# Kernel optimization log

Hardware: AMD Instinct MI355X
Metric: run time of the kernel (lower is better)

The kernel has to match this reference:

```python
import jax, jax.numpy as jnp
import numpy as np

N, L, P = 32, 512, 256
H, E = 8, 128          # n_head, n_emb; d_model = H*E = 1024
NEG = -1e20            # self.eps2 mask fill


def gelu(v):
    # torch F.gelu default = exact erf gelu
    return jax.nn.gelu(v, approximate=False)


def setup_inputs() -> dict:
    key = jax.random.key(0)
    ks = jax.random.split(key, 10)
    s = 0.05
    x = jax.random.normal(ks[0], (N, L, H * E), dtype=jnp.float32)
    hyper_adj = (jax.random.uniform(ks[1], (N, L, P)) < 0.1).astype(jnp.float32)
    W1 = jax.random.normal(ks[2], (E, E), dtype=jnp.float32) * s
    b1 = jax.random.normal(ks[3], (E,), dtype=jnp.float32) * s
    W2 = jax.random.normal(ks[4], (E,), dtype=jnp.float32) * s
    b2 = jax.random.normal(ks[5], (), dtype=jnp.float32) * s
    W3 = jax.random.normal(ks[6], (E, E), dtype=jnp.float32) * s
    b3 = jax.random.normal(ks[7], (E,), dtype=jnp.float32) * s
    W4 = jax.random.normal(ks[8], (2 * E,), dtype=jnp.float32) * s
    b4 = jax.random.normal(ks[9], (), dtype=jnp.float32) * s
    return {"x": x, "hyper_adj": hyper_adj, "W1": W1, "b1": b1, "W2": W2,
            "b2": b2, "W3": W3, "b3": b3, "W4": W4, "b4": b4}


def reference(x, hyper_adj, W1, b1, W2, b2, W3, b3, W4, b4):
    n, l, d = x.shape
    # (N, H, L, E)
    xh = x.reshape(n, l, H, E).transpose(0, 2, 1, 3)
    xh = jnp.einsum('nhle,ef->nhlf', xh, W1) + b1              # hyper_linear1
    mask = hyper_adj[:, None, :, :] != 0.0                      # (N,1,L,P), bcast over H
    # node -> edge attention: score per node broadcast over P, masked, softmax over heads (dim=1)
    xv = gelu(xh) @ W2 + b2                                     # (N,H,L)  hyper_linear2
    x_value = jnp.where(mask, xv[..., None], NEG)               # (N,H,L,P)
    att_edge = jax.nn.softmax(x_value, axis=1)
    hyper_edge = gelu(jnp.einsum('nhlp,nhle->nhpe', att_edge, xh))
    hyper_edge = jnp.einsum('nhpe,ef->nhpf', hyper_edge, W3) + b3  # hyper_linear3
    # edge -> node attention; linear4(gelu(cat(he, x))) decomposed (gelu elementwise)
    a_edge = gelu(hyper_edge) @ W4[:E]                          # (N,H,P)
    a_node = gelu(xh) @ W4[E:]                                  # (N,H,L)
    e_values = a_node[:, :, :, None] + a_edge[:, :, None, :] + b4  # (N,H,L,P)
    e_values = jnp.where(mask, e_values, NEG)
    att_node = jax.nn.softmax(e_values, axis=1)
    x_nodes = jnp.einsum('nhlp,nhpe->nhle', att_node, hyper_edge)
    out = gelu(x_nodes).transpose(0, 2, 1, 3).reshape(n, l, d)
    # scatter overwrite: nodes in no hyperedge keep their input
    no_edge = (jnp.sum(hyper_adj, axis=-1) == 0.0)[..., None]   # (N,L,1)
    return jnp.where(no_edge, x, out)
```

## Files before the change

### kernel.cpp

```cpp
#include <hip/hip_runtime.h>
#include <math.h>

#define NB 32
#define LL 512
#define PP 256
#define HH 8
#define EE 128
#define DD 1024

typedef __attribute__((ext_vector_type(4))) float f32x4;
typedef __attribute__((ext_vector_type(8))) short short8;

__device__ __forceinline__ float rcp_f(float v) {
    float r; asm("v_rcp_f32 %0, %1" : "=v"(r) : "v"(v)); return r;
}
__device__ __forceinline__ float gelu_f(float v) {
    float z = v * (1.5957691216f + 0.0713548163f * v * v);
    float e = __expf(-z);
    return v * rcp_f(1.0f + e);
}
__device__ __forceinline__ unsigned short bf16_rne(float v) {
    unsigned u = __float_as_uint(v);
    unsigned r = u + 0x7FFFu + ((u >> 16) & 1u);
    return (unsigned short)(r >> 16);
}
__device__ __forceinline__ float bf2f(short s) {
    return __uint_as_float(((unsigned)(unsigned short)s) << 16);
}

__global__ __launch_bounds__(256) void kpack(const float* __restrict__ W1,
                                             const float* __restrict__ W3,
                                             unsigned short* __restrict__ W1h,
                                             unsigned short* __restrict__ W1l,
                                             unsigned short* __restrict__ W3h,
                                             unsigned short* __restrict__ W3l) {
    const float* W = blockIdx.x ? W3 : W1;
    unsigned short* Ph = blockIdx.x ? W3h : W1h;
    unsigned short* Pl = blockIdx.x ? W3l : W1l;
    for (int i = threadIdx.x; i < 16384; i += 256) {
        int oct = i >> 10, col = (i >> 3) & 127, j = i & 7;
        float v = W[(oct * 8 + j) * 128 + col];
        unsigned short hb = bf16_rne(v);
        float hf = __uint_as_float((unsigned)hb << 16);
        Ph[i] = hb;
        Pl[i] = bf16_rne(v - hf);
    }
}

__global__ __launch_bounds__(256) void k0_bits(const float* __restrict__ adj,
                                               unsigned* __restrict__ bits,
                                               unsigned* __restrict__ bitsT,
                                               unsigned* __restrict__ flags) {
    __shared__ unsigned lbits[64][8];
    int n  = blockIdx.x >> 3;
    int l0 = (blockIdx.x & 7) * 64;
    int lane = threadIdx.x & 63;
    int wv   = threadIdx.x >> 6;
    for (int r = wv; r < 64; r += 4) {
        int l = l0 + r;
        const float* row = adj + ((size_t)n * LL + l) * PP;
        int cnt = 0;
        for (int c = 0; c < 4; ++c) {
            float v = row[c * 64 + lane];
            unsigned long long b = __ballot(v != 0.0f);
            if (lane == 0) {
                lbits[r][c * 2]     = (unsigned)b;
                lbits[r][c * 2 + 1] = (unsigned)(b >> 32);
                cnt += __popcll(b);
            }
        }
        if (lane == 0) {
            flags[n * LL + l] = (cnt == 0) ? 1u : 0u;
            for (int w = 0; w < 8; ++w)
                bits[((size_t)n * LL + l) * 8 + w] = lbits[r][w];
        }
    }
    __syncthreads();
    int p = threadIdx.x;
    unsigned w0 = 0, w1 = 0;
    int wp = p >> 5, bp = p & 31;
    for (int j = 0; j < 32; ++j) {
        w0 |= ((lbits[j][wp] >> bp) & 1u) << j;
        w1 |= ((lbits[j + 32][wp] >> bp) & 1u) << j;
    }
    bitsT[((size_t)n * PP + p) * 16 + (l0 >> 5)]     = w0;
    bitsT[((size_t)n * PP + p) * 16 + (l0 >> 5) + 1] = w1;
}

__global__ __launch_bounds__(512) void gemm1c(const float* __restrict__ A,
                                              const unsigned short* __restrict__ Bhi,
                                              const float* __restrict__ bias,
                                              const float* __restrict__ W2,
                                              const float* __restrict__ W4,
                                              unsigned short* __restrict__ xhb,
                                              unsigned short* __restrict__ sb,
                                              float* __restrict__ eu) {
    __shared__ __align__(16) char buf[32768];
    __shared__ float rs4[4][64][2];
    __shared__ float rs[64][2];
    float* As = (float*)buf;
    unsigned short* tbuf = (unsigned short*)buf;
    int tid = threadIdx.x, lane = tid & 63, w = tid >> 6;
    int b = blockIdx.x;
    size_t blockRow0 = (size_t)b * 64;
    int rl = lane & 15, g = lane >> 4;
    int mt = w & 3, eh = w >> 2;

    {
        const f32x4* Ag = (const f32x4*)(A + blockRow0 * 128);
        #pragma unroll
        for (int i = 0; i < 4; ++i) {
            int idx = i * 512 + tid;
            int row = idx >> 5, c4 = idx & 31;
            f32x4 v = Ag[idx];
            *(f32x4*)((char*)As + ((row * 512 + c4 * 16) ^ ((row & 7) << 5))) = v;
        }
    }
    __syncthreads();

    f32x4 acc[4];
    #pragma unroll
    for (int nt = 0; nt < 4; ++nt) acc[nt] = (f32x4){0.f, 0.f, 0.f, 0.f};

    #pragma unroll
    for (int kc = 0; kc < 4; ++kc) {
        short8 ah;
        {
            int arow = mt * 16 + rl;
            int cb = (kc * 32 + g * 8) * 4;
            int sw = (arow & 7) << 5;
            f32x4 a0 = *(const f32x4*)((char*)As + ((arow * 512 + cb) ^ sw));
            f32x4 a1 = *(const f32x4*)((char*)As + ((arow * 512 + cb + 16) ^ sw));
            ah[0] = (short)bf16_rne(a0.x); ah[1] = (short)bf16_rne(a0.y);
            ah[2] = (short)bf16_rne(a0.z); ah[3] = (short)bf16_rne(a0.w);
            ah[4] = (short)bf16_rne(a1.x); ah[5] = (short)bf16_rne(a1.y);
            ah[6] = (short)bf16_rne(a1.z); ah[7] = (short)bf16_rne(a1.w);
        }
        #pragma unroll
        for (int ntl = 0; ntl < 4; ++ntl) {
            int oct = kc * 4 + g, col = eh * 64 + ntl * 16 + rl;
            short8 bh = *(const short8*)(Bhi + ((size_t)(oct * 128 + col)) * 8);
            acc[ntl] = __builtin_amdgcn_mfma_f32_16x16x32_bf16(ah, bh, acc[ntl], 0, 0, 0);
        }
    }
    __syncthreads();

    {
        int l_loc = mt * 2 + (g >> 1);
        int hbase2 = (g & 1) * 8;
        #pragma unroll
        for (int ntl = 0; ntl < 4; ++ntl) {
            int col = eh * 64 + ntl * 16 + rl;
            float bv = bias[col];
            ushort4 o;
            o.x = bf16_rne(acc[ntl][0] + bv);
            o.y = bf16_rne(acc[ntl][1] + bv);
            o.z = bf16_rne(acc[ntl][2] + bv);
            o.w = bf16_rne(acc[ntl][3] + bv);
            *(ushort4*)((char*)tbuf + (l_loc * 2048 + col * 16 + hbase2)) = o;
        }
    }
    __syncthreads();

    {
        int ec = tid & 15, l_loc = (tid >> 4) & 7, eq = tid >> 7;
        float xv_p[8] = {0,0,0,0,0,0,0,0};
        float an_p[8] = {0,0,0,0,0,0,0,0};
        #pragma unroll
        for (int i = 0; i < 2; ++i) {
            int e = (eq * 2 + i) * 16 + ec;
            short8 v = *(const short8*)((char*)tbuf + (l_loc * 2048 + e * 16));
            float w2 = W2[e], w4 = W4[128 + e];
            #pragma unroll
            for (int h = 0; h < 8; ++h) {
                float gv = gelu_f(bf2f(v[h]));
                xv_p[h] += gv * w2;
                an_p[h] += gv * w4;
            }
        }
        #pragma unroll
        for (int h = 0; h < 8; ++h) {
            #pragma unroll
            for (int m = 1; m < 16; m <<= 1) {
                xv_p[h] += __shfl_xor(xv_p[h], m);
                an_p[h] += __shfl_xor(an_p[h], m);
            }
        }
        if (ec == 0) {
            #pragma unroll
            for (int h = 0; h < 8; ++h) {
                rs4[eq][l_loc * 8 + h][0] = xv_p[h];
                rs4[eq][l_loc * 8 + h][1] = an_p[h];
            }
        }
    }

    int n = b >> 6, kg = b & 63;
    #pragma unroll
    for (int rep = 0; rep < 2; ++rep) {
        int id = rep * 512 + tid;
        int h = id >> 7, e = id & 127;
        short8 v;
        #pragma unroll
        for (int j = 0; j < 8; ++j)
            v[j] = (short)*(const unsigned short*)((char*)tbuf + (j * 2048 + e * 16 + h * 2));
        *(short8*)(xhb + ((size_t)(n * 8 + h)) * 65536 + (size_t)(kg * 128 + e) * 8) = v;
    }
    __syncthreads();

    if (tid < 64) {
        rs[tid][0] = rs4[0][tid][0] + rs4[1][tid][0] + rs4[2][tid][0] + rs4[3][tid][0];
        rs[tid][1] = rs4[0][tid][1] + rs4[1][tid][1] + rs4[2][tid][1] + rs4[3][tid][1];
    }
    __syncthreads();
    if (tid < 8) {
        int l = kg * 8 + tid;
        float xv[8], an[8];
        #pragma unroll
        for (int h = 0; h < 8; ++h) { xv[h] = rs[tid * 8 + h][0]; an[h] = rs[tid * 8 + h][1]; }
        float mx = xv[0];
        #pragma unroll
        for (int h = 1; h < 8; ++h) mx = fmaxf(mx, xv[h]);
        float ex[8], ssum = 0.f;
        #pragma unroll
        for (int h = 0; h < 8; ++h) { ex[h] = expf(xv[h] - mx); ssum += ex[h]; }
        float inv = 1.0f / ssum;
        #pragma unroll
        for (int h = 0; h < 8; ++h)
            sb[((size_t)(n * 8 + h)) * 512 + l] = bf16_rne(ex[h] * inv);
        float mxa = an[0];
        #pragma unroll
        for (int h = 1; h < 8; ++h) mxa = fmaxf(mxa, an[h]);
        f32x4 e0, e1;
        #pragma unroll
        for (int h = 0; h < 4; ++h) e0[h] = expf(an[h] - mxa);
        #pragma unroll
        for (int h = 0; h < 4; ++h) e1[h] = expf(an[4 + h] - mxa);
        float* ep = eu + ((size_t)(n * 512 + l)) * 8;
        *(f32x4*)ep = e0;
        *(f32x4*)(ep + 4) = e1;
    }
}

__global__ __launch_bounds__(1024) void k23_fused(const unsigned short* __restrict__ xhb,
                                                  const unsigned short* __restrict__ s_in,
                                                  const unsigned* __restrict__ bitsT,
                                                  const unsigned short* __restrict__ W3h,
                                                  const float* __restrict__ b3,
                                                  const float* __restrict__ W4,
                                                  unsigned short* __restrict__ heT,
                                                  float* __restrict__ ev) {
    __shared__ __align__(16) unsigned short kpk[65536];
    __shared__ unsigned bT_s[16 * 256];
    __shared__ __align__(16) unsigned short smb_s[512];
    __shared__ float rs_ae[256][2];
    int bh = blockIdx.x;
    int n = bh >> 3, h = bh & 7;
    int tid = threadIdx.x, lane = tid & 63, w = tid >> 6;
    int rl = lane & 15, g = lane >> 4;

    {
        int p = tid >> 2, q = tid & 3;
        uint4 wds = *(const uint4*)(bitsT + ((size_t)(n * 256 + p)) * 16 + q * 4);
        bT_s[(q * 4 + 0) * 256 + p] = wds.x;
        bT_s[(q * 4 + 1) * 256 + p] = wds.y;
        bT_s[(q * 4 + 2) * 256 + p] = wds.z;
        bT_s[(q * 4 + 3) * 256 + p] = wds.w;
    }
    if (tid < 512) smb_s[tid] = s_in[(size_t)bh * 512 + tid];
    {
        const unsigned short* xb = xhb + (size_t)bh * 65536;
        #pragma unroll
        for (int rep = 0; rep < 8; ++rep) {
            int idx = rep * 1024 + tid;
            *(short8*)&kpk[idx * 8] = *(const short8*)(xb + (size_t)idx * 8);
        }
    }
    __syncthreads();

    int wm = w & 7, wn = w >> 3;
    f32x4 acc[2][4];
    #pragma unroll
    for (int i = 0; i < 2; ++i)
        #pragma unroll
        for (int nt = 0; nt < 4; ++nt) acc[i][nt] = (f32x4){0.f, 0.f, 0.f, 0.f};

    for (int kt = 0; kt < 16; ++kt) {
        short8 sv = *(const short8*)&smb_s[kt * 32 + g * 8];
        short8 bfr[4];
        #pragma unroll
        for (int nt = 0; nt < 4; ++nt)
            bfr[nt] = *(const short8*)&kpk[(((kt * 4 + g) << 7) + wn * 64 + nt * 16 + rl) * 8];
        #pragma unroll
        for (int i = 0; i < 2; ++i) {
            unsigned word = bT_s[kt * 256 + (wm * 2 + i) * 16 + rl];
            unsigned byte = (word >> (g * 8)) & 255u;
            short8 af;
            #pragma unroll
            for (int j = 0; j < 8; ++j)
                af[j] = ((byte >> j) & 1u) ? sv[j] : (short)0x3E00;
            #pragma unroll
            for (int nt = 0; nt < 4; ++nt)
                acc[i][nt] = __builtin_amdgcn_mfma_f32_16x16x32_bf16(af, bfr[nt], acc[i][nt], 0, 0, 0);
        }
    }
    __syncthreads();

    char* A2  = (char*)kpk;
    char* tb2 = (char*)kpk + 65536;

    #pragma unroll
    for (int i = 0; i < 2; ++i)
        #pragma unroll
        for (int nt = 0; nt < 4; ++nt) {
            int e = wn * 64 + nt * 16 + rl;
            #pragma unroll
            for (int r = 0; r < 4; ++r) {
                int p = (wm * 2 + i) * 16 + g * 4 + r;
                *(unsigned short*)(A2 + ((p * 256 + e * 2) ^ ((p & 15) << 4))) =
                    bf16_rne(gelu_f(acc[i][nt][r]));
            }
        }
    __syncthreads();

    f32x4 acc2[2][4];
    #pragma unroll
    for (int i = 0; i < 2; ++i)
        #pragma unroll
        for (int nt = 0; nt < 4; ++nt) acc2[i][nt] = (f32x4){0.f, 0.f, 0.f, 0.f};

    #pragma unroll
    for (int kt2 = 0; kt2 < 4; ++kt2) {
        short8 af2[2];
        #pragma unroll
        for (int i = 0; i < 2; ++i) {
            int p = (wm * 2 + i) * 16 + rl;
            af2[i] = *(const short8*)(A2 + ((p * 256 + (kt2 * 32 + g * 8) * 2) ^ ((p & 15) << 4)));
        }
        #pragma unroll
        for (int nt = 0; nt < 4; ++nt) {
            int oct = kt2 * 4 + g, col = (wn * 4 + nt) * 16 + rl;
            short8 bhv = *(const short8*)(W3h + ((size_t)(oct * 128 + col)) * 8);
            #pragma unroll
            for (int i = 0; i < 2; ++i)
                acc2[i][nt] = __builtin_amdgcn_mfma_f32_16x16x32_bf16(af2[i], bhv, acc2[i][nt], 0, 0, 0);
        }
    }

    float ae_p[2][4] = {{0.f,0.f,0.f,0.f},{0.f,0.f,0.f,0.f}};
    #pragma unroll
    for (int nt = 0; nt < 4; ++nt) {
        int f = (wn * 4 + nt) * 16 + rl;
        float bv = b3[f], w4v = W4[f];
        #pragma unroll
        for (int i = 0; i < 2; ++i) {
            float v0 = acc2[i][nt][0] + bv;
            float v1 = acc2[i][nt][1] + bv;
            float v2 = acc2[i][nt][2] + bv;
            float v3 = acc2[i][nt][3] + bv;
            ae_p[i][0] += gelu_f(v0) * w4v;
            ae_p[i][1] += gelu_f(v1) * w4v;
            ae_p[i][2] += gelu_f(v2) * w4v;
            ae_p[i][3] += gelu_f(v3) * w4v;
            int p0 = (wm * 2 + i) * 16 + g * 4;
            int byte = (f * 512 + p0 * 2) ^ ((f & 7) << 4);
            *(ushort4*)(tb2 + byte) =
                make_ushort4(bf16_rne(v0), bf16_rne(v1), bf16_rne(v2), bf16_rne(v3));
        }
    }
    #pragma unroll
    for (int i = 0; i < 2; ++i)
        #pragma unroll
        for (int r = 0; r < 4; ++r) {
            float a = ae_p[i][r];
            a += __shfl_xor(a, 1); a += __shfl_xor(a, 2); a += __shfl_xor(a, 4); a += __shfl_xor(a, 8);
            if (rl == 0) rs_ae[(wm * 2 + i) * 16 + g * 4 + r][wn] = a;
        }
    __syncthreads();

    unsigned short* ho = heT + (size_t)bh * 32768;
    #pragma unroll
    for (int rep = 0; rep < 4; ++rep) {
        int id = rep * 1024 + tid;
        int f = id >> 5, pj = id & 31;
        int byte = (f * 512 + pj * 16) ^ ((f & 7) << 4);
        short8 v = *(const short8*)(tb2 + byte);
        *(short8*)(ho + (size_t)f * 256 + pj * 8) = v;
    }
    if (tid < 256) {
        float ae = rs_ae[tid][0] + rs_ae[tid][1];
        ev[((size_t)(n * 256 + tid)) * 8 + h] = expf(ae);
    }
}

__global__ __launch_bounds__(256) void k4_dense(const float* __restrict__ eu,
                                                const float* __restrict__ ev,
                                                const unsigned* __restrict__ bits,
                                                unsigned short* __restrict__ rdm) {
    __shared__ float ev_t[256][8];
    int b = blockIdx.x;
    int n = b >> 3, l0 = (b & 7) * 64;
    int tid = threadIdx.x;
    {
        const f32x4* src = (const f32x4*)(ev + (size_t)n * 2048);
        f32x4* dst = (f32x4*)&ev_t[0][0];
        dst[tid] = src[tid];
        dst[tid + 256] = src[tid + 256];
    }
    __syncthreads();
    int l = l0 + (tid >> 2), pq = tid & 3;
    size_t rowg = (size_t)n * 512 + l;
    f32x4 ea = *(const f32x4*)(eu + rowg * 8);
    f32x4 eb = *(const f32x4*)(eu + rowg * 8 + 4);
    unsigned w0 = bits[rowg * 8 + pq * 2], w1 = bits[rowg * 8 + pq * 2 + 1];
    for (int c = 0; c < 8; ++c) {
        short8 o8;
        #pragma unroll
        for (int k = 0; k < 8; ++k) {
            int pl = c * 8 + k;
            int p = pq * 64 + pl;
            f32x4 va = *(const f32x4*)&ev_t[p][0];
            f32x4 vb = *(const f32x4*)&ev_t[p][4];
            float den = ea.x * va.x + ea.y * va.y + ea.z * va.z + ea.w * va.w
                      + eb.x * vb.x + eb.y * vb.y + eb.z * vb.z + eb.w * vb.w;
            unsigned bit = (pl < 32) ? ((w0 >> pl) & 1u) : ((w1 >> (pl - 32)) & 1u);
            float r = bit ? rcp_f(den) : 0.0f;
            o8[k] = (short)bf16_rne(r);
        }
        *(short8*)(rdm + rowg * 256 + pq * 64 + c * 8) = o8;
    }
}

__global__ __launch_bounds__(1024) void k5_mfma(const unsigned short* __restrict__ heT,
                                                const unsigned short* __restrict__ rdm,
                                                const float* __restrict__ eu,
                                                const float* __restrict__ ev,
                                                const unsigned* __restrict__ flags,
                                                const float* __restrict__ x,
                                                float* __restrict__ out) {
    __shared__ __align__(16) unsigned short heT_s[128 * 256];
    __shared__ __align__(16) unsigned short A_s[64 * 256];
    __shared__ float evh_s[256];
    __shared__ float euh_s[64];
    __shared__ float cs_s[128];
    __shared__ float csr_s[4][128];
    __shared__ unsigned flg_s[64];

    int bid = blockIdx.x;
    int xcd = bid & 7, slot = bid >> 3;
    int n = xcd * 4 + (slot & 3), h = slot >> 2;
    int bh = n * 8 + h;
    int tid = threadIdx.x, lane = tid & 63, w = tid >> 6;

    const unsigned short* hb = heT + (size_t)bh * 32768;
    #pragma unroll
    for (int i = 0; i < 4; ++i) {
        int id = tid + i * 1024;
        int e = id >> 5, jj = id & 31;
        short8 v = *(const short8*)(hb + e * 256 + jj * 8);
        *(short8*)((char*)heT_s + ((e * 512 + jj * 16) ^ ((e & 7) << 4))) = v;
    }
    if (tid < 256) evh_s[tid] = ev[((size_t)(n * 256 + tid)) * 8 + h];
    __syncthreads();
    if (tid < 512) {
        int e = tid & 127, q = tid >> 7;
        float a = 0.f;
        #pragma unroll
        for (int j = 0; j < 8; ++j) {
            int byte = (e * 512 + (q * 64 + j * 8) * 2) ^ ((e & 7) << 4);
            short8 v = *(const short8*)((char*)heT_s + byte);
            #pragma unroll
            for (int k = 0; k < 8; ++k) a += bf2f(v[k]);
        }
        csr_s[q][e] = a;
    }
    __syncthreads();
    if (tid < 128) cs_s[tid] = 0.125f * (csr_s[0][tid] + csr_s[1][tid] + csr_s[2][tid] + csr_s[3][tid]);

    int rl = lane & 15, g = lane >> 4;
    int wm = w & 3, wn = w >> 2;
    int swz = (rl & 7) << 4;

    for (int lt = 0; lt < 8; ++lt) {
        int l0 = lt * 64;
        if (tid < 64) {
            euh_s[tid] = eu[((size_t)(n * 512 + l0 + tid)) * 8 + h];
            flg_s[tid] = flags[n * 512 + l0 + tid];
        }
        __syncthreads();
        {
            int l_loc = tid >> 4, p8 = (tid & 15) * 16;
            float euh = euh_s[l_loc];
            const unsigned short* rp = rdm + ((size_t)(n * 512 + l0 + l_loc)) * 256 + p8;
            #pragma unroll
            for (int c = 0; c < 2; ++c) {
                short8 rv = *(const short8*)(rp + c * 8);
                short8 o8;
                #pragma unroll
                for (int k = 0; k < 8; ++k) {
                    unsigned u = (unsigned)(unsigned short)rv[k];
                    float rf = __uint_as_float(u << 16);
                    float m125 = (u != 0u) ? -0.125f : 0.0f;
                    float a = fmaf(euh * evh_s[p8 + c * 8 + k], rf, m125);
                    o8[k] = (short)bf16_rne(a);
                }
                *(short8*)((char*)A_s + ((l_loc * 512 + (p8 + c * 8) * 2) ^ ((l_loc & 7) << 4))) = o8;
            }
        }
        __syncthreads();
        f32x4 acc[2];
        acc[0] = (f32x4){0.f, 0.f, 0.f, 0.f};
        acc[1] = (f32x4){0.f, 0.f, 0.f, 0.f};
        #pragma unroll
        for (int kt = 0; kt < 8; ++kt) {
            int arow = wm * 16 + rl;
            short8 af = *(const short8*)((char*)A_s + ((arow * 512 + kt * 64 + g * 16) ^ swz));
            short8 b0, b1;
            {
                int e0 = wn * 32 + rl;
                int e1 = wn * 32 + 16 + rl;
                b0 = *(const short8*)((char*)heT_s + ((e0 * 512 + kt * 64 + g * 16) ^ swz));
                b1 = *(const short8*)((char*)heT_s + ((e1 * 512 + kt * 64 + g * 16) ^ swz));
            }
            acc[0] = __builtin_amdgcn_mfma_f32_16x16x32_bf16(af, b0, acc[0], 0, 0, 0);
            acc[1] = __builtin_amdgcn_mfma_f32_16x16x32_bf16(af, b1, acc[1], 0, 0, 0);
        }
        #pragma unroll
        for (int j = 0; j < 2; ++j) {
            int e = wn * 32 + j * 16 + rl;
            float csv = cs_s[e];
            #pragma unroll
            for (int r = 0; r < 4; ++r) {
                int row = wm * 16 + g * 4 + r;
                int l = l0 + row;
                size_t addr = ((size_t)(n * 512 + l)) * 1024 + h * 128 + e;
                if (flg_s[row]) {
                    out[addr] = x[addr];
                } else {
                    out[addr] = gelu_f(acc[j][r] + csv);
                }
            }
        }
        __syncthreads();
    }
}

extern "C" void kernel_launch(void* const* d_in, const int* in_sizes, int n_in,
                              void* d_out, int out_size, void* d_ws, size_t ws_size,
                              hipStream_t stream) {
    (void)in_sizes; (void)n_in; (void)out_size; (void)ws_size;
    const float* x   = (const float*)d_in[0];
    const float* adj = (const float*)d_in[1];
    const float* W1  = (const float*)d_in[2];
    const float* b1  = (const float*)d_in[3];
    const float* W2  = (const float*)d_in[4];
    const float* W3  = (const float*)d_in[6];
    const float* b3  = (const float*)d_in[7];
    const float* W4  = (const float*)d_in[8];
    float* out = (float*)d_out;

    char* ws = (char*)d_ws;
    size_t off = 0;
    auto alloc = [&](size_t bytes) -> void* {
        void* p = ws + off;
        off += (bytes + 255) & ~(size_t)255;
        return p;
    };
    unsigned short* xhb = (unsigned short*)alloc((size_t)NB * HH * 65536 * 2);
    unsigned short* sb  = (unsigned short*)alloc((size_t)NB * HH * LL * 2);
    float* eu   = (float*)alloc((size_t)NB * LL * HH * 4);
    float* ev   = (float*)alloc((size_t)NB * PP * HH * 4);
    unsigned short* heT = (unsigned short*)alloc((size_t)NB * HH * EE * PP * 2);
    unsigned short* rdm = (unsigned short*)alloc((size_t)NB * LL * PP * 2);
    unsigned* bits  = (unsigned*)alloc((size_t)NB * LL * 8 * 4);
    unsigned* bitsT = (unsigned*)alloc((size_t)NB * PP * 16 * 4);
    unsigned* flags = (unsigned*)alloc((size_t)NB * LL * 4);
    unsigned short* W1h = (unsigned short*)alloc(16384 * 2);
    unsigned short* W1l = (unsigned short*)alloc(16384 * 2);
    unsigned short* W3h = (unsigned short*)alloc(16384 * 2);
    unsigned short* W3l = (unsigned short*)alloc(16384 * 2);

    hipLaunchKernelGGL(kpack, dim3(2), dim3(256), 0, stream, W1, W3, W1h, W1l, W3h, W3l);
    hipLaunchKernelGGL(k0_bits, dim3(NB * 8), dim3(256), 0, stream, adj, bits, bitsT, flags);
    hipLaunchKernelGGL(gemm1c, dim3(2048), dim3(512), 0, stream, x, W1h, b1, W2, W4, xhb, sb, eu);
    hipLaunchKernelGGL(k23_fused, dim3(NB * HH), dim3(1024), 0, stream, xhb, sb, bitsT, W3h, b3, W4, heT, ev);
    hipLaunchKernelGGL(k4_dense, dim3(NB * 8), dim3(256), 0, stream, eu, ev, bits, rdm);
    hipLaunchKernelGGL(k5_mfma, dim3(NB * HH), dim3(1024), 0, stream, heT, rdm, eu, ev, flags, x, out);
}
```

Measured before the change: 142.1 us.

## Split k5 E dimension into two halves to halve LDS tile footprint

The k5_mfma kernel now processes the 128-wide E dimension in two passes of 64 columns. This halves the shared-memory buffer holding the hyper-edge tile and the column-sum scratch. The goal is to cut LDS usage so more blocks can be resident per CU. In exchange, each block rebuilds the attention A tile from rdm, eu and ev twice and runs twice as many L-tile loops and barriers, with half the MFMA work per wave per tile.

Result: slower. 160.3 us (+12.8%).

```diff
diff --git a/kernel.cpp b/kernel.cpp
--- a/kernel.cpp
+++ b/kernel.cpp
@@ -438,12 +438,12 @@
                                                 const unsigned* __restrict__ flags,
                                                 const float* __restrict__ x,
                                                 float* __restrict__ out) {
-    __shared__ __align__(16) unsigned short heT_s[128 * 256];
+    __shared__ __align__(16) unsigned short heT_s[64 * 256];
     __shared__ __align__(16) unsigned short A_s[64 * 256];
     __shared__ float evh_s[256];
     __shared__ float euh_s[64];
-    __shared__ float cs_s[128];
-    __shared__ float csr_s[4][128];
+    __shared__ float cs_s[64];
+    __shared__ float csr_s[8][64];
     __shared__ unsigned flg_s[64];
 
     int bid = blockIdx.x;
@@ -451,97 +451,99 @@
     int n = xcd * 4 + (slot & 3), h = slot >> 2;
     int bh = n * 8 + h;
     int tid = threadIdx.x, lane = tid & 63, w = tid >> 6;
-
-    const unsigned short* hb = heT + (size_t)bh * 32768;
-    #pragma unroll
-    for (int i = 0; i < 4; ++i) {
-        int id = tid + i * 1024;
-        int e = id >> 5, jj = id & 31;
-        short8 v = *(const short8*)(hb + e * 256 + jj * 8);
-        *(short8*)((char*)heT_s + ((e * 512 + jj * 16) ^ ((e & 7) << 4))) = v;
-    }
-    if (tid < 256) evh_s[tid] = ev[((size_t)(n * 256 + tid)) * 8 + h];
-    __syncthreads();
-    if (tid < 512) {
-        int e = tid & 127, q = tid >> 7;
-        float a = 0.f;
-        #pragma unroll
-        for (int j = 0; j < 8; ++j) {
-            int byte = (e * 512 + (q * 64 + j * 8) * 2) ^ ((e & 7) << 4);
-            short8 v = *(const short8*)((char*)heT_s + byte);
-            #pragma unroll
-            for (int k = 0; k < 8; ++k) a += bf2f(v[k]);
-        }
-        csr_s[q][e] = a;
-    }
-    __syncthreads();
-    if (tid < 128) cs_s[tid] = 0.125f * (csr_s[0][tid] + csr_s[1][tid] + csr_s[2][tid] + csr_s[3][tid]);
-
     int rl = lane & 15, g = lane >> 4;
     int wm = w & 3, wn = w >> 2;
     int swz = (rl & 7) << 4;
 
-    for (int lt = 0; lt < 8; ++lt) {
-        int l0 = lt * 64;
-        if (tid < 64) {
-            euh_s[tid] = eu[((size_t)(n * 512 + l0 + tid)) * 8 + h];
-            flg_s[tid] = flags[n * 512 + l0 + tid];
-        }
+    if (tid < 256) evh_s[tid] = ev[((size_t)(n * 256 + tid)) * 8 + h];
+
+    for (int eh2 = 0; eh2 < 2; ++eh2) {
         __syncthreads();
         {
-            int l_loc = tid >> 4, p8 = (tid & 15) * 16;
-            float euh = euh_s[l_loc];
-            const unsigned short* rp = rdm + ((size_t)(n * 512 + l0 + l_loc)) * 256 + p8;
-            #pragma unroll
-            for (int c = 0; c < 2; ++c) {
-                short8 rv = *(const short8*)(rp + c * 8);
-                short8 o8;
+            const unsigned short* hb = heT + (size_t)bh * 32768 + (size_t)eh2 * 64 * 256;
+            #pragma unroll
+            for (int i = 0; i < 2; ++i) {
+                int id = tid + i * 1024;
+                int e = id >> 5, jj = id & 31;
+                short8 v = *(const short8*)(hb + e * 256 + jj * 8);
+                *(short8*)((char*)heT_s + ((e * 512 + jj * 16) ^ ((e & 7) << 4))) = v;
+            }
+        }
+        __syncthreads();
+        if (tid < 512) {
+            int e = tid & 63, q = tid >> 6;
+            float a = 0.f;
+            #pragma unroll
+            for (int j = 0; j < 4; ++j) {
+                int byte = (e * 512 + (q * 32 + j * 8) * 2) ^ ((e & 7) << 4);
+                short8 v = *(const short8*)((char*)heT_s + byte);
                 #pragma unroll
-                for (int k = 0; k < 8; ++k) {
-                    unsigned u = (unsigned)(unsigned short)rv[k];
-                    float rf = __uint_as_float(u << 16);
-                    float m125 = (u != 0u) ? -0.125f : 0.0f;
-                    float a = fmaf(euh * evh_s[p8 + c * 8 + k], rf, m125);
-                    o8[k] = (short)bf16_rne(a);
+                for (int k = 0; k < 8; ++k) a += bf2f(v[k]);
+            }
+            csr_s[q][e] = a;
+        }
+        __syncthreads();
+        if (tid < 64) {
+            float a = 0.f;
+            #pragma unroll
+            for (int q = 0; q < 8; ++q) a += csr_s[q][tid];
+            cs_s[tid] = 0.125f * a;
+        }
+
+        for (int lt = 0; lt < 8; ++lt) {
+            int l0 = lt * 64;
+            if (tid < 64) {
+                euh_s[tid] = eu[((size_t)(n * 512 + l0 + tid)) * 8 + h];
+                flg_s[tid] = flags[n * 512 + l0 + tid];
+            }
+            __syncthreads();
+            {
+                int l_loc = tid >> 4, p8 = (tid & 15) * 16;
+                float euh = euh_s[l_loc];
+                const unsigned short* rp = rdm + ((size_t)(n * 512 + l0 + l_loc)) * 256 + p8;
+                #pragma unroll
+                for (int c = 0; c < 2; ++c) {
+                    short8 rv = *(const short8*)(rp + c * 8);
+                    short8 o8;
+                    #pragma unroll
+                    for (int k = 0; k < 8; ++k) {
+                        unsigned u = (unsigned)(unsigned short)rv[k];
+                        float rf = __uint_as_float(u << 16);
+                        float m125 = (u != 0u) ? -0.125f : 0.0f;
+                        float a = fmaf(euh * evh_s[p8 + c * 8 + k], rf, m125);
+                        o8[k] = (short)bf16_rne(a);
+                    }
+                    *(short8*)((char*)A_s + ((l_loc * 512 + (p8 + c * 8) * 2) ^ ((l_loc & 7) << 4))) = o8;
                 }
-                *(short8*)((char*)A_s + ((l_loc * 512 + (p8 + c * 8) * 2) ^ ((l_loc & 7) << 4))) = o8;
-            }
-        }
-        __syncthreads();
-        f32x4 acc[2];
-        acc[0] = (f32x4){0.f, 0.f, 0.f, 0.f};
-        acc[1] = (f32x4){0.f, 0.f, 0.f, 0.f};
-        #pragma unroll
-        for (int kt = 0; kt < 8; ++kt) {
-            int arow = wm * 16 + rl;
-            short8 af = *(const short8*)((char*)A_s + ((arow * 512 + kt * 64 + g * 16) ^ swz));
-            short8 b0, b1;
+            }
+            __syncthreads();
+            f32x4 acc = (f32x4){0.f, 0.f, 0.f, 0.f};
+            #pragma unroll
+            for (int kt = 0; kt < 8; ++kt) {
+                int arow = wm * 16 + rl;
+                short8 af = *(const short8*)((char*)A_s + ((arow * 512 + kt * 64 + g * 16) ^ swz));
+                int e0 = wn * 16 + rl;
+                short8 b0 = *(const short8*)((char*)heT_s + ((e0 * 512 + kt * 64 + g * 16) ^ swz));
+                acc = __builtin_amdgcn_mfma_f32_16x16x32_bf16(af, b0, acc, 0, 0, 0);
+            }
             {
-                int e0 = wn * 32 + rl;
-                int e1 = wn * 32 + 16 + rl;
-                b0 = *(const short8*)((char*)heT_s + ((e0 * 512 + kt * 64 + g * 16) ^ swz));
-                b1 = *(const short8*)((char*)heT_s + ((e1 * 512 + kt * 64 + g * 16) ^ swz));
-            }
-            acc[0] = __builtin_amdgcn_mfma_f32_16x16x32_bf16(af, b0, acc[0], 0, 0, 0);
-            acc[1] = __builtin_amdgcn_mfma_f32_16x16x32_bf16(af, b1, acc[1], 0, 0, 0);
-        }
-        #pragma unroll
-        for (int j = 0; j < 2; ++j) {
-            int e = wn * 32 + j * 16 + rl;
-            float csv = cs_s[e];
-            #pragma unroll
-            for (int r = 0; r < 4; ++r) {
-                int row = wm * 16 + g * 4 + r;
-                int l = l0 + row;
-                size_t addr = ((size_t)(n * 512 + l)) * 1024 + h * 128 + e;
-                if (flg_s[row]) {
-                    out[addr] = x[addr];
-                } else {
-                    out[addr] = gelu_f(acc[j][r] + csv);
+                int e_loc = wn * 16 + rl;
+                int e = eh2 * 64 + e_loc;
+                float csv = cs_s[e_loc];
+                #pragma unroll
+                for (int r = 0; r < 4; ++r) {
+                    int row = wm * 16 + g * 4 + r;
+                    int l = l0 + row;
+                    size_t addr = ((size_t)(n * 512 + l)) * 1024 + h * 128 + e;
+                    if (flg_s[row]) {
+                        out[addr] = x[addr];
+                    } else {
+                        out[addr] = gelu_f(acc[r] + csv);
+                    }
                 }
             }
-        }
-        __syncthreads();
+            __syncthreads();
+        }
     }
 }
 
```
